# Kernel tuning notes

Hardware: AMD Instinct MI355X
Metric: run time of the kernel (lower is better)

## Reference

```python
import jax, jax.numpy as jnp
import numpy as np

B, W, D, R = 2, 1024, 1024, 16
GAMMA_FLOOR = 0.85


def setup_inputs() -> dict:
    key = jax.random.key(0)
    ks = jax.random.split(key, 8)
    h = jax.random.normal(ks[0], (B, W, D), jnp.float32)
    # faithful parameter initialization (as in __init__)
    gammas = jnp.linspace(0.95, 0.995, R)
    decay_logit = jnp.log(gammas / (1.0 - gammas))
    pos = jnp.arange(W, dtype=jnp.float32)
    causal = jnp.tril(jnp.ones((W, W), jnp.float32))
    dist0 = jnp.clip(pos[None, :] - pos[:, None], 0.0)  # (j - i)+ , used for k_base init
    k_init = jnp.exp(-0.15 * dist0) * causal
    k_base = k_init / jnp.clip(k_init.sum(axis=1, keepdims=True), 1e-8)
    u = jax.random.normal(ks[1], (D, R), jnp.float32) * 0.05
    v = jax.random.normal(ks[2], (D, R), jnp.float32) * 0.05
    proj_w = jax.random.normal(ks[3], (D, D), jnp.float32) * 0.02
    proj_b = jnp.zeros((D,), jnp.float32)
    up_w = jax.random.normal(ks[4], (D, 2 * D), jnp.float32) * 0.02
    up_b = jnp.zeros((2 * D,), jnp.float32)
    down_w = jax.random.normal(ks[5], (2 * D, D), jnp.float32) * 0.02
    down_b = jnp.zeros((D,), jnp.float32)
    return {
        'h': h,
        'decay_logit': decay_logit,
        'k_base': k_base,
        'k_base_gate_logit': jnp.asarray(8.0, jnp.float32),
        'u': u,
        'v': v,
        'alpha_logit': jnp.asarray(0.0, jnp.float32),
        'proj_w': proj_w,
        'proj_b': proj_b,
        'norm1_scale': jnp.ones((D,), jnp.float32),
        'norm2_scale': jnp.ones((D,), jnp.float32),
        'up_w': up_w,
        'up_b': up_b,
        'down_w': down_w,
        'down_b': down_b,
    }


def _rmsnorm(x, scale, eps=1e-8):
    return x / jnp.sqrt(jnp.mean(x * x, axis=-1, keepdims=True) + eps) * scale


def _l2norm(x, eps=1e-8):
    # matches F.normalize: x / max(||x||, eps)
    n = jnp.sqrt(jnp.sum(x * x, axis=-1, keepdims=True))
    return x / jnp.maximum(n, eps)


def reference(h, decay_logit, k_base, k_base_gate_logit, u, v, alpha_logit,
              proj_w, proj_b, norm1_scale, norm2_scale, up_w, up_b, down_w, down_b):
    b, w, d = h.shape
    pos = jnp.arange(w, dtype=h.dtype)
    causal = jnp.tril(jnp.ones((w, w), h.dtype))

    residual = h
    h_norm = _rmsnorm(h, norm1_scale)

    gate = jax.nn.sigmoid(k_base_gate_logit)
    kb = k_base[:w, :w] * causal * gate
    out = jnp.einsum('ij,bjd->bid', kb, h_norm)

    q = _l2norm(h_norm @ u)  # (b, w, r)
    k = _l2norm(h_norm @ v)  # (b, w, r)

    gamma = GAMMA_FLOOR + (1.0 - GAMMA_FLOOR) * jax.nn.sigmoid(decay_logit)  # (r,)
    alpha = jax.nn.sigmoid(alpha_logit)  # alpha_cap = 1.0

    # decay mask: exp((i-j)+ * log(gamma_r)) on causal entries -> (w, w, r)
    dist = jnp.clip(pos[:, None] - pos[None, :], 0.0)
    log_gamma = jnp.log(jnp.clip(gamma, 1e-8))
    decay_mask = jnp.exp(dist[:, :, None] * log_gamma[None, None, :]) * causal[:, :, None]

    kh = k[..., None] * h_norm[:, :, None, :]  # (b, w, r, d)
    causal_inner = jnp.einsum('ijr,bjrd->bird', decay_mask, kh)  # (b, w, r, d)
    out = out + alpha * jnp.einsum('bwr,bwrd->bwd', q, causal_inner)

    out = out @ proj_w + proj_b
    h2 = residual + out
    h2n = _rmsnorm(h2, norm2_scale)
    mlp = jax.nn.gelu(h2n @ up_w + up_b, approximate=False) @ down_w + down_b
    return h2 + mlp
```

## Files before the change

kernel.cpp:

```cpp
#include <hip/hip_runtime.h>

#define Bv 2
#define Wv 1024
#define Dv 1024
#define Rv 16

typedef __bf16 bf16;
typedef __attribute__((ext_vector_type(8))) __bf16 bf16x8;
typedef __attribute__((ext_vector_type(4))) __bf16 bf16x4;
typedef __attribute__((ext_vector_type(4))) float f32x4;

static __device__ __forceinline__ float sigmoidf_(float x) {
    return 1.0f / (1.0f + expf(-x));
}

static __device__ __forceinline__ void gload_lds16(const void* g, void* l) {
    __builtin_amdgcn_global_load_lds(
        (const __attribute__((address_space(1))) unsigned int*)g,
        (__attribute__((address_space(3))) unsigned int*)l, 16, 0, 0);
}

__global__ void rmsnorm_kernel(const float* __restrict__ x,
                               const float* __restrict__ scale,
                               bf16* __restrict__ outb) {
    int row = blockIdx.x;
    int t = threadIdx.x;
    float4 v = *(const float4*)(x + (size_t)row * Dv + t * 4);
    float ss = v.x * v.x + v.y * v.y + v.z * v.z + v.w * v.w;
    for (int off = 32; off > 0; off >>= 1) ss += __shfl_down(ss, off);
    __shared__ float wsum[4];
    __shared__ float inv_s;
    int lane = t & 63, wid = t >> 6;
    if (lane == 0) wsum[wid] = ss;
    __syncthreads();
    if (t == 0) {
        float tot = wsum[0] + wsum[1] + wsum[2] + wsum[3];
        inv_s = rsqrtf(tot * (1.0f / Dv) + 1e-8f);
    }
    __syncthreads();
    float inv = inv_s;
    float4 sc = *(const float4*)(scale + t * 4);
    bf16x4 ob = {(bf16)(v.x * inv * sc.x), (bf16)(v.y * inv * sc.y),
                 (bf16)(v.z * inv * sc.z), (bf16)(v.w * inv * sc.w)};
    *(bf16x4*)(outb + (size_t)row * Dv + t * 4) = ob;
}

__global__ void inv2_kernel(const bf16* __restrict__ x, float* __restrict__ inv2g) {
    int row = blockIdx.x;
    int t = threadIdx.x;
    bf16x4 vb = *(const bf16x4*)(x + (size_t)row * Dv + t * 4);
    float a0 = (float)vb[0], a1 = (float)vb[1], a2 = (float)vb[2], a3 = (float)vb[3];
    float ss = a0 * a0 + a1 * a1 + a2 * a2 + a3 * a3;
    for (int off = 32; off > 0; off >>= 1) ss += __shfl_down(ss, off);
    __shared__ float wsum[4];
    int lane = t & 63, wid = t >> 6;
    if (lane == 0) wsum[wid] = ss;
    __syncthreads();
    if (t == 0) {
        float tot = wsum[0] + wsum[1] + wsum[2] + wsum[3];
        inv2g[row] = rsqrtf(tot * (1.0f / Dv) + 1e-8f);
    }
}

__global__ void prep_kernel(const float* __restrict__ proj_w, const float* __restrict__ up_w,
                            const float* __restrict__ down_w,
                            const float* __restrict__ u, const float* __restrict__ v,
                            const float* __restrict__ n2,
                            const bf16* __restrict__ hnb,
                            bf16* __restrict__ proj_wT, bf16* __restrict__ up_wT,
                            bf16* __restrict__ down_wT, bf16* __restrict__ h_normT,
                            bf16* __restrict__ uvT) {
    __shared__ float tile[32][33];
    int blk = blockIdx.x;
    int t = threadIdx.x;
    if (blk >= 7168) {
        int i = (blk - 7168) * 256 + t;
        int rcol = i >> 10, d = i & (Wv - 1);
        float val = (rcol < Rv) ? u[(size_t)d * Rv + rcol] : v[(size_t)d * Rv + (rcol - Rv)];
        uvT[i] = (bf16)val;
        return;
    }
    const void* src;
    const float* rscale = nullptr;
    bf16* dst;
    int rows, cols, r0, c0;
    bool f32src = true;
    if (blk < 1024) {
        src = proj_w; dst = proj_wT; rows = 1024; cols = 1024;
        c0 = (blk & 31) * 32; r0 = (blk >> 5) * 32;
    } else if (blk < 3072) {
        int idx = blk - 1024;
        src = up_w; dst = up_wT; rows = 1024; cols = 2048; rscale = n2;
        c0 = (idx & 63) * 32; r0 = (idx >> 6) * 32;
    } else if (blk < 5120) {
        int idx = blk - 3072;
        src = down_w; dst = down_wT; rows = 2048; cols = 1024;
        c0 = (idx & 31) * 32; r0 = (idx >> 5) * 32;
    } else {
        int idx = blk - 5120;
        int b = idx >> 10; idx &= 1023;
        src = hnb + (size_t)b * Wv * Dv; dst = h_normT + (size_t)b * Dv * Wv;
        rows = 1024; cols = 1024; f32src = false;
        c0 = (idx & 31) * 32; r0 = (idx >> 5) * 32;
    }
    int r = t >> 3, c4 = (t & 7) * 4;
    float vv[4];
    if (f32src) {
        float4 x = *(const float4*)((const float*)src + (size_t)(r0 + r) * cols + c0 + c4);
        vv[0] = x.x; vv[1] = x.y; vv[2] = x.z; vv[3] = x.w;
    } else {
        bf16x4 x = *(const bf16x4*)((const bf16*)src + (size_t)(r0 + r) * cols + c0 + c4);
        vv[0] = (float)x[0]; vv[1] = (float)x[1]; vv[2] = (float)x[2]; vv[3] = (float)x[3];
    }
    float sc = rscale ? rscale[r0 + r] : 1.0f;
    tile[r][c4 + 0] = vv[0] * sc;
    tile[r][c4 + 1] = vv[1] * sc;
    tile[r][c4 + 2] = vv[2] * sc;
    tile[r][c4 + 3] = vv[3] * sc;
    __syncthreads();
    int n = t >> 3, k4 = (t & 7) * 4;
    bf16x4 ob = {(bf16)tile[k4 + 0][n], (bf16)tile[k4 + 1][n],
                 (bf16)tile[k4 + 2][n], (bf16)tile[k4 + 3][n]};
    *(bf16x4*)(dst + (size_t)(c0 + n) * rows + r0 + k4) = ob;
}

__global__ __launch_bounds__(256) void qk_mfma(
    const bf16* __restrict__ hnb,
    const bf16* __restrict__ uvT,
    const float* __restrict__ decay_logit,
    bf16* __restrict__ Qs, bf16* __restrict__ Ks) {
    int t = threadIdx.x, lane = t & 63, wid = t >> 6;
    int wm = wid >> 1, wn = wid & 1;
    int row0 = blockIdx.x * 32 + wm * 16;
    const bf16* Arow = hnb + (size_t)(row0 + (lane & 15)) * Dv + (lane >> 4) * 8;
    const bf16* Brow = uvT + (size_t)(wn * 16 + (lane & 15)) * Dv + (lane >> 4) * 8;
    f32x4 acc = {};
#pragma unroll 8
    for (int k0 = 0; k0 < Dv; k0 += 32) {
        bf16x8 a = *(const bf16x8*)(Arow + k0);
        bf16x8 b = *(const bf16x8*)(Brow + k0);
        acc = __builtin_amdgcn_mfma_f32_16x16x32_bf16(a, b, acc, 0, 0, 0);
    }
    int col = lane & 15;
    float dl = decay_logit[col];
    float gamma = 0.85f + 0.15f * sigmoidf_(dl);
    float logg = log2f(gamma);
#pragma unroll
    for (int r = 0; r < 4; ++r) {
        float vv = acc[r];
        float ss = vv * vv;
#pragma unroll
        for (int m = 1; m < 16; m <<= 1) ss += __shfl_xor(ss, m);
        float nrm = fmaxf(sqrtf(ss), 1e-8f);
        float val = vv / nrm;
        int grow = row0 + (lane >> 4) * 4 + r;
        int i = grow & (Wv - 1);
        if (wn == 0) {
            float pw = exp2f((float)i * logg);
            Qs[(size_t)grow * Rv + col] = (bf16)(val * pw);
        } else {
            float pwi = exp2f(-(float)i * logg);
            Ks[(size_t)grow * Rv + col] = (bf16)(val * pwi);
        }
    }
}

__global__ __launch_bounds__(256) void sbuild_mfma(
    const bf16* __restrict__ Qs, const bf16* __restrict__ Ks,
    const float* __restrict__ kbase,
    const float* __restrict__ gate_logit,
    const float* __restrict__ alpha_logit,
    bf16* __restrict__ S) {
    int it = blockIdx.y, jt = blockIdx.x;
    if (jt > it) return;
    int b = blockIdx.z;
    int t = threadIdx.x, lane = t & 63, wid = t >> 6;
    int wm = wid >> 1, wn = wid & 1;
    int i0 = it * 64, j0 = jt * 64;
    int l15 = lane & 15, chunk = lane >> 4;
    bf16x8 af[2], bfr[2];
    bf16x8 z8 = {};
#pragma unroll
    for (int mi = 0; mi < 2; ++mi)
        af[mi] = (chunk < 2)
            ? *(const bf16x8*)(Qs + (size_t)(b * Wv + i0 + wm * 32 + mi * 16 + l15) * Rv + chunk * 8)
            : z8;
#pragma unroll
    for (int ni = 0; ni < 2; ++ni)
        bfr[ni] = (chunk < 2)
            ? *(const bf16x8*)(Ks + (size_t)(b * Wv + j0 + wn * 32 + ni * 16 + l15) * Rv + chunk * 8)
            : z8;
    f32x4 acc[2][2] = {};
#pragma unroll
    for (int mi = 0; mi < 2; ++mi)
#pragma unroll
        for (int ni = 0; ni < 2; ++ni)
            acc[mi][ni] = __builtin_amdgcn_mfma_f32_16x16x32_bf16(af[mi], bfr[ni], acc[mi][ni], 0, 0, 0);
    float gate = sigmoidf_(gate_logit[0]);
    float alpha = sigmoidf_(alpha_logit[0]);
#pragma unroll
    for (int mi = 0; mi < 2; ++mi)
#pragma unroll
        for (int ni = 0; ni < 2; ++ni) {
            int j = j0 + wn * 32 + ni * 16 + l15;
#pragma unroll
            for (int r = 0; r < 4; ++r) {
                int i = i0 + wm * 32 + mi * 16 + chunk * 4 + r;
                float s = (j <= i) ? gate * kbase[(size_t)i * Wv + j] + alpha * acc[mi][ni][r] : 0.f;
                S[((size_t)b * Wv + i) * Wv + j] = (bf16)s;
            }
        }
}

template <bool GELU, bool OUT_BF16, int RES, bool CAUSAL, bool RS>
__global__ __launch_bounds__(256, 3) void mfma_gemm(
    const bf16* __restrict__ A, const bf16* __restrict__ Bt,
    const float* __restrict__ bias, const void* __restrict__ res,
    const float* __restrict__ rowscale,
    void* __restrict__ Cout, int M, int N, int K,
    long sA, long sB, long sC) {
    constexpr int BM = 64, BN = 64, BK = 128;
    __shared__ bf16 As[BM * BK];
    __shared__ bf16 Bs[BN * BK];

    const int gx = gridDim.x, gy = gridDim.y;
    int flat = blockIdx.x + gx * (blockIdx.y + gy * blockIdx.z);
    const int nwg = gx * gy * gridDim.z;
    const int cpx = nwg >> 3;
    int swz = (flat & 7) * cpx + (flat >> 3);
    const int bx = swz % gx;
    int tmp = swz / gx;
    const int by = tmp % gy;
    const int bz = tmp / gy;

    A += (size_t)bz * sA;
    Bt += (size_t)bz * sB;
    const int m0 = by * BM, n0 = bx * BN;
    const int t = threadIdx.x;
    const int lane = t & 63, wid = t >> 6;
    const int wm = wid >> 1, wn = wid & 1;
    f32x4 acc[2][2] = {};

    const int Klim = CAUSAL ? (m0 + BM < K ? m0 + BM : K) : K;

    const int srow = t >> 4;
    const int fcs = (t & 15) ^ (srow & 7);

    const int q = lane >> 4, s = lane & 7, l15 = lane & 15;

    for (int k0 = 0; k0 < Klim; k0 += BK) {
        __syncthreads();
#pragma unroll
        for (int it = 0; it < 4; ++it) {
            int r = srow + it * 16;
            gload_lds16(A + (size_t)(m0 + r) * K + k0 + fcs * 8,
                        As + it * 2048 + wid * 512);
        }
#pragma unroll
        for (int it = 0; it < 4; ++it) {
            int r = srow + it * 16;
            gload_lds16(Bt + (size_t)(n0 + r) * K + k0 + fcs * 8,
                        Bs + it * 2048 + wid * 512);
        }
        __syncthreads();

        bf16x8 af[2][4], bfr[2][4];
#pragma unroll
        for (int mi = 0; mi < 2; ++mi)
#pragma unroll
            for (int kk = 0; kk < 4; ++kk) {
                af[mi][kk] = *(const bf16x8*)&As[(wm * 32 + mi * 16 + l15) * BK + (((kk * 4 + q) ^ s) * 8)];
                bfr[mi][kk] = *(const bf16x8*)&Bs[(wn * 32 + mi * 16 + l15) * BK + (((kk * 4 + q) ^ s) * 8)];
            }
#pragma unroll
        for (int kk = 0; kk < 4; ++kk)
#pragma unroll
            for (int mi = 0; mi < 2; ++mi)
#pragma unroll
                for (int ni = 0; ni < 2; ++ni)
                    acc[mi][ni] = __builtin_amdgcn_mfma_f32_16x16x32_bf16(
                        af[mi][kk], bfr[ni][kk], acc[mi][ni], 0, 0, 0);
    }

    const int row_base = m0 + wm * 32;
    const int col_base = n0 + wn * 32;
#pragma unroll
    for (int mi = 0; mi < 2; ++mi) {
#pragma unroll
        for (int ni = 0; ni < 2; ++ni) {
            int col = col_base + ni * 16 + l15;
            float bv = bias ? bias[col] : 0.f;
#pragma unroll
            for (int r = 0; r < 4; ++r) {
                int row = row_base + mi * 16 + q * 4 + r;
                float val = acc[mi][ni][r];
                if (RS) val *= rowscale[row];
                val += bv;
                if (GELU) val = 0.5f * val * (1.0f + erff(val * 0.7071067811865476f));
                if (RES == 1)
                    val += ((const float*)res)[(size_t)bz * sC + (size_t)row * N + col];
                else if (RES == 2)
                    val += (float)((const bf16*)res)[(size_t)bz * sC + (size_t)row * N + col];
                if (OUT_BF16)
                    ((bf16*)Cout)[(size_t)bz * sC + (size_t)row * N + col] = (bf16)val;
                else
                    ((float*)Cout)[(size_t)bz * sC + (size_t)row * N + col] = val;
            }
        }
    }
}

extern "C" void kernel_launch(void* const* d_in, const int* in_sizes, int n_in,
                              void* d_out, int out_size, void* d_ws, size_t ws_size,
                              hipStream_t stream) {
    const float* h = (const float*)d_in[0];
    const float* decay_logit = (const float*)d_in[1];
    const float* k_base = (const float*)d_in[2];
    const float* gate_logit = (const float*)d_in[3];
    const float* u = (const float*)d_in[4];
    const float* v = (const float*)d_in[5];
    const float* alpha_logit = (const float*)d_in[6];
    const float* proj_w = (const float*)d_in[7];
    const float* proj_b = (const float*)d_in[8];
    const float* n1 = (const float*)d_in[9];
    const float* n2 = (const float*)d_in[10];
    const float* up_w = (const float*)d_in[11];
    const float* up_b = (const float*)d_in[12];
    const float* down_w = (const float*)d_in[13];
    const float* down_b = (const float*)d_in[14];
    float* out = (float*)d_out;

    char* ws = (char*)d_ws;
    bf16* hnb = (bf16*)ws;        ws += (size_t)Bv * Wv * Dv * 2;
    bf16* h_normT = (bf16*)ws;    ws += (size_t)Bv * Dv * Wv * 2;
    bf16* uvT = (bf16*)ws;        ws += (size_t)32 * Wv * 2;
    bf16* Qs = (bf16*)ws;         ws += (size_t)Bv * Wv * Rv * 2;
    bf16* Ks = (bf16*)ws;         ws += (size_t)Bv * Wv * Rv * 2;
    float* inv2g = (float*)ws;    ws += (size_t)Bv * Wv * 4;
    bf16* S = (bf16*)ws;          ws += (size_t)Bv * Wv * Wv * 2;
    bf16* out_s = (bf16*)ws;      ws += (size_t)Bv * Wv * Dv * 2;
    bf16* h2b = (bf16*)ws;        ws += (size_t)Bv * Wv * Dv * 2;
    bf16* g = (bf16*)ws;          ws += (size_t)Bv * Wv * 2 * Dv * 2;
    bf16* proj_wT = (bf16*)ws;    ws += (size_t)Dv * Dv * 2;
    bf16* up_wT = (bf16*)ws;      ws += (size_t)2 * Dv * Dv * 2;
    bf16* down_wT = (bf16*)ws;    ws += (size_t)2 * Dv * Dv * 2;

    int rows = Bv * Wv;

    rmsnorm_kernel<<<rows, 256, 0, stream>>>(h, n1, hnb);
    prep_kernel<<<7296, 256, 0, stream>>>(proj_w, up_w, down_w, u, v, n2, hnb,
                                          proj_wT, up_wT, down_wT, h_normT, uvT);
    qk_mfma<<<rows / 32, 256, 0, stream>>>(hnb, uvT, decay_logit, Qs, Ks);
    sbuild_mfma<<<dim3(Wv / 64, Wv / 64, Bv), 256, 0, stream>>>(
        Qs, Ks, k_base, gate_logit, alpha_logit, S);
    mfma_gemm<false, true, 0, true, false><<<dim3(Dv / 64, Wv / 64, Bv), 256, 0, stream>>>(
        S, h_normT, nullptr, nullptr, nullptr, out_s, Wv, Dv, Wv,
        (long)Wv * Wv, (long)Dv * Wv, (long)Wv * Dv);
    mfma_gemm<false, true, 1, false, false><<<dim3(Dv / 64, rows / 64, 1), 256, 0, stream>>>(
        out_s, proj_wT, proj_b, h, nullptr, h2b, rows, Dv, Dv, 0, 0, 0);
    inv2_kernel<<<rows, 256, 0, stream>>>(h2b, inv2g);
    mfma_gemm<true, true, 0, false, true><<<dim3(2 * Dv / 64, rows / 64, 1), 256, 0, stream>>>(
        h2b, up_wT, up_b, nullptr, inv2g, g, rows, 2 * Dv, Dv, 0, 0, 0);
    mfma_gemm<false, false, 2, false, false><<<dim3(Dv / 64, rows / 64, 1), 256, 0, stream>>>(
        g, down_wT, down_b, h2b, nullptr, out, rows, Dv, 2 * Dv, 0, 0, 0);
}
```

Before: 97.44 us.

## Use single-wave 64x64 GEMM blocks with double-buffered async LDS loads

Rewrites the shared GEMM kernel so each 64x64 output tile is computed by one 64-lane wavefront instead of four waves. The kernel now double-buffers LDS with BK=64 and prefetches two stages ahead using global_load_lds, replacing __syncthreads with explicit vmcnt/lgkmcnt waits. The aim is to overlap global loads with MFMA work and drop block-wide barriers. In exchange, each wave holds a 4x4 accumulator tile (more registers) and per-block parallelism falls to a quarter. The redundant reload of the last tile at the loop tail adds wasted loads.

```diff
diff --git a/kernel.cpp b/kernel.cpp
--- a/kernel.cpp
+++ b/kernel.cpp
@@ -213,15 +213,15 @@
 }
 
 template <bool GELU, bool OUT_BF16, int RES, bool CAUSAL, bool RS>
-__global__ __launch_bounds__(256, 3) void mfma_gemm(
+__global__ __launch_bounds__(64) void mfma_gemm(
     const bf16* __restrict__ A, const bf16* __restrict__ Bt,
     const float* __restrict__ bias, const void* __restrict__ res,
     const float* __restrict__ rowscale,
     void* __restrict__ Cout, int M, int N, int K,
     long sA, long sB, long sC) {
-    constexpr int BM = 64, BN = 64, BK = 128;
-    __shared__ bf16 As[BM * BK];
-    __shared__ bf16 Bs[BN * BK];
+    constexpr int BK = 64;
+    __shared__ bf16 As[2][64 * BK];
+    __shared__ bf16 Bs[2][64 * BK];
 
     const int gx = gridDim.x, gy = gridDim.y;
     int flat = blockIdx.x + gx * (blockIdx.y + gy * blockIdx.z);
@@ -235,64 +235,70 @@
 
     A += (size_t)bz * sA;
     Bt += (size_t)bz * sB;
-    const int m0 = by * BM, n0 = bx * BN;
+    const int m0 = by * 64, n0 = bx * 64;
     const int t = threadIdx.x;
-    const int lane = t & 63, wid = t >> 6;
-    const int wm = wid >> 1, wn = wid & 1;
-    f32x4 acc[2][2] = {};
-
-    const int Klim = CAUSAL ? (m0 + BM < K ? m0 + BM : K) : K;
-
-    const int srow = t >> 4;
-    const int fcs = (t & 15) ^ (srow & 7);
-
-    const int q = lane >> 4, s = lane & 7, l15 = lane & 15;
-
-    for (int k0 = 0; k0 < Klim; k0 += BK) {
-        __syncthreads();
-#pragma unroll
-        for (int it = 0; it < 4; ++it) {
-            int r = srow + it * 16;
-            gload_lds16(A + (size_t)(m0 + r) * K + k0 + fcs * 8,
-                        As + it * 2048 + wid * 512);
+
+    f32x4 acc[4][4] = {};
+
+    const int Klim = CAUSAL ? (m0 + 64 < K ? m0 + 64 : K) : K;
+    const int nt = Klim >> 6;
+
+    const int srow = t >> 3;
+    const int sg = (t & 7) ^ srow;
+    const bf16* Asrc = A + (size_t)(m0 + srow) * K + sg * 8;
+    const bf16* Bsrc = Bt + (size_t)(n0 + srow) * K + sg * 8;
+
+    const int q = t >> 4, s = t & 7, l15 = t & 15;
+
+#define STAGE(sb, kt)                                                          \
+    do {                                                                       \
+        const bf16* a_ = Asrc + (size_t)(kt) * BK;                             \
+        const bf16* b_ = Bsrc + (size_t)(kt) * BK;                             \
+        _Pragma("unroll") for (int it_ = 0; it_ < 8; ++it_) {                  \
+            gload_lds16(a_ + (size_t)it_ * 8 * K, &As[sb][it_ * 512]);         \
+            gload_lds16(b_ + (size_t)it_ * 8 * K, &Bs[sb][it_ * 512]);         \
+        }                                                                      \
+    } while (0)
+
+    STAGE(0, 0);
+    STAGE(1, nt > 1 ? 1 : 0);
+
+    for (int tt = 0; tt < nt; ++tt) {
+        const int cur = tt & 1;
+        asm volatile("s_waitcnt vmcnt(16)" ::: "memory");
+
+#pragma unroll
+        for (int kk = 0; kk < 2; ++kk) {
+            bf16x8 af[4], bfr[4];
+#pragma unroll
+            for (int mi = 0; mi < 4; ++mi)
+                af[mi] = *(const bf16x8*)&As[cur][(mi * 16 + l15) * BK + (((kk * 4 + q) ^ s) * 8)];
+#pragma unroll
+            for (int ni = 0; ni < 4; ++ni)
+                bfr[ni] = *(const bf16x8*)&Bs[cur][(ni * 16 + l15) * BK + (((kk * 4 + q) ^ s) * 8)];
+#pragma unroll
+            for (int mi = 0; mi < 4; ++mi)
+#pragma unroll
+                for (int ni = 0; ni < 4; ++ni)
+                    acc[mi][ni] = __builtin_amdgcn_mfma_f32_16x16x32_bf16(
+                        af[mi], bfr[ni], acc[mi][ni], 0, 0, 0);
         }
-#pragma unroll
-        for (int it = 0; it < 4; ++it) {
-            int r = srow + it * 16;
-            gload_lds16(Bt + (size_t)(n0 + r) * K + k0 + fcs * 8,
-                        Bs + it * 2048 + wid * 512);
-        }
-        __syncthreads();
-
-        bf16x8 af[2][4], bfr[2][4];
-#pragma unroll
-        for (int mi = 0; mi < 2; ++mi)
-#pragma unroll
-            for (int kk = 0; kk < 4; ++kk) {
-                af[mi][kk] = *(const bf16x8*)&As[(wm * 32 + mi * 16 + l15) * BK + (((kk * 4 + q) ^ s) * 8)];
-                bfr[mi][kk] = *(const bf16x8*)&Bs[(wn * 32 + mi * 16 + l15) * BK + (((kk * 4 + q) ^ s) * 8)];
-            }
-#pragma unroll
-        for (int kk = 0; kk < 4; ++kk)
-#pragma unroll
-            for (int mi = 0; mi < 2; ++mi)
-#pragma unroll
-                for (int ni = 0; ni < 2; ++ni)
-                    acc[mi][ni] = __builtin_amdgcn_mfma_f32_16x16x32_bf16(
-                        af[mi][kk], bfr[ni][kk], acc[mi][ni], 0, 0, 0);
-    }
-
-    const int row_base = m0 + wm * 32;
-    const int col_base = n0 + wn * 32;
-#pragma unroll
-    for (int mi = 0; mi < 2; ++mi) {
-#pragma unroll
-        for (int ni = 0; ni < 2; ++ni) {
-            int col = col_base + ni * 16 + l15;
+
+        asm volatile("s_waitcnt lgkmcnt(0)" ::: "memory");
+        int kn = (tt + 2 < nt) ? tt + 2 : nt - 1;
+        STAGE(cur, kn);
+    }
+#undef STAGE
+
+#pragma unroll
+    for (int mi = 0; mi < 4; ++mi) {
+#pragma unroll
+        for (int ni = 0; ni < 4; ++ni) {
+            int col = n0 + ni * 16 + l15;
             float bv = bias ? bias[col] : 0.f;
 #pragma unroll
             for (int r = 0; r < 4; ++r) {
-                int row = row_base + mi * 16 + q * 4 + r;
+                int row = m0 + mi * 16 + q * 4 + r;
                 float val = acc[mi][ni][r];
                 if (RS) val *= rowscale[row];
                 val += bv;
@@ -353,14 +359,14 @@
     qk_mfma<<<rows / 32, 256, 0, stream>>>(hnb, uvT, decay_logit, Qs, Ks);
     sbuild_mfma<<<dim3(Wv / 64, Wv / 64, Bv), 256, 0, stream>>>(
         Qs, Ks, k_base, gate_logit, alpha_logit, S);
-    mfma_gemm<false, true, 0, true, false><<<dim3(Dv / 64, Wv / 64, Bv), 256, 0, stream>>>(
+    mfma_gemm<false, true, 0, true, false><<<dim3(Dv / 64, Wv / 64, Bv), 64, 0, stream>>>(
         S, h_normT, nullptr, nullptr, nullptr, out_s, Wv, Dv, Wv,
         (long)Wv * Wv, (long)Dv * Wv, (long)Wv * Dv);
-    mfma_gemm<false, true, 1, false, false><<<dim3(Dv / 64, rows / 64, 1), 256, 0, stream>>>(
+    mfma_gemm<false, true, 1, false, false><<<dim3(Dv / 64, rows / 64, 1), 64, 0, stream>>>(
         out_s, proj_wT, proj_b, h, nullptr, h2b, rows, Dv, Dv, 0, 0, 0);
     inv2_kernel<<<rows, 256, 0, stream>>>(h2b, inv2g);
-    mfma_gemm<true, true, 0, false, true><<<dim3(2 * Dv / 64, rows / 64, 1), 256, 0, stream>>>(
+    mfma_gemm<true, true, 0, false, true><<<dim3(2 * Dv / 64, rows / 64, 1), 64, 0, stream>>>(
         h2b, up_wT, up_b, nullptr, inv2g, g, rows, 2 * Dv, Dv, 0, 0, 0);
-    mfma_gemm<false, false, 2, false, false><<<dim3(Dv / 64, rows / 64, 1), 256, 0, stream>>>(
+    mfma_gemm<false, false, 2, false, false><<<dim3(Dv / 64, rows / 64, 1), 64, 0, stream>>>(
         g, down_wT, down_b, h2b, nullptr, out, rows, Dv, 2 * Dv, 0, 0, 0);
 }
```

After: 134.2 us. 37.8% more time.

## Fuse S-matrix construction into causal GEMM and fuse RMSNorm reduction into epilogue

Applied to the files above, without the earlier changes.

Removes the separate kernel that materialised the full bf16 S matrix. The causal GEMM now computes each S tile on the fly from Q/K MFMAs and a bf16 copy of k_base, writing it straight into LDS. The second RMSNorm kernel is also dropped: the proj GEMM epilogue writes partial row sums of squares, and the up-projection GEMM reduces them into per-row inverse scales. This saves a 4 MB write and reread of S plus two launches. In exchange, S is recomputed by every column-tile block (16x redundant small MFMAs and k_base reads), and k_base is converted to bf16 in the prep kernel, which is extra precision loss.

```diff
diff --git a/kernel.cpp b/kernel.cpp
--- a/kernel.cpp
+++ b/kernel.cpp
@@ -45,34 +45,25 @@
     *(bf16x4*)(outb + (size_t)row * Dv + t * 4) = ob;
 }
 
-__global__ void inv2_kernel(const bf16* __restrict__ x, float* __restrict__ inv2g) {
-    int row = blockIdx.x;
-    int t = threadIdx.x;
-    bf16x4 vb = *(const bf16x4*)(x + (size_t)row * Dv + t * 4);
-    float a0 = (float)vb[0], a1 = (float)vb[1], a2 = (float)vb[2], a3 = (float)vb[3];
-    float ss = a0 * a0 + a1 * a1 + a2 * a2 + a3 * a3;
-    for (int off = 32; off > 0; off >>= 1) ss += __shfl_down(ss, off);
-    __shared__ float wsum[4];
-    int lane = t & 63, wid = t >> 6;
-    if (lane == 0) wsum[wid] = ss;
-    __syncthreads();
-    if (t == 0) {
-        float tot = wsum[0] + wsum[1] + wsum[2] + wsum[3];
-        inv2g[row] = rsqrtf(tot * (1.0f / Dv) + 1e-8f);
-    }
-}
-
 __global__ void prep_kernel(const float* __restrict__ proj_w, const float* __restrict__ up_w,
                             const float* __restrict__ down_w,
                             const float* __restrict__ u, const float* __restrict__ v,
                             const float* __restrict__ n2,
+                            const float* __restrict__ kbase,
                             const bf16* __restrict__ hnb,
                             bf16* __restrict__ proj_wT, bf16* __restrict__ up_wT,
                             bf16* __restrict__ down_wT, bf16* __restrict__ h_normT,
-                            bf16* __restrict__ uvT) {
+                            bf16* __restrict__ uvT, bf16* __restrict__ kbb) {
     __shared__ float tile[32][33];
     int blk = blockIdx.x;
     int t = threadIdx.x;
+    if (blk >= 7296) {
+        size_t base = (size_t)(blk - 7296) * 1024 + t * 4;
+        float4 x = *(const float4*)(kbase + base);
+        bf16x4 ob = {(bf16)x.x, (bf16)x.y, (bf16)x.z, (bf16)x.w};
+        *(bf16x4*)(kbb + base) = ob;
+        return;
+    }
     if (blk >= 7168) {
         int i = (blk - 7168) * 256 + t;
         int rcol = i >> 10, d = i & (Wv - 1);
@@ -165,63 +156,15 @@
     }
 }
 
-__global__ __launch_bounds__(256) void sbuild_mfma(
+__global__ __launch_bounds__(256, 3) void sgemm1(
     const bf16* __restrict__ Qs, const bf16* __restrict__ Ks,
-    const float* __restrict__ kbase,
-    const float* __restrict__ gate_logit,
-    const float* __restrict__ alpha_logit,
-    bf16* __restrict__ S) {
-    int it = blockIdx.y, jt = blockIdx.x;
-    if (jt > it) return;
-    int b = blockIdx.z;
-    int t = threadIdx.x, lane = t & 63, wid = t >> 6;
-    int wm = wid >> 1, wn = wid & 1;
-    int i0 = it * 64, j0 = jt * 64;
-    int l15 = lane & 15, chunk = lane >> 4;
-    bf16x8 af[2], bfr[2];
-    bf16x8 z8 = {};
-#pragma unroll
-    for (int mi = 0; mi < 2; ++mi)
-        af[mi] = (chunk < 2)
-            ? *(const bf16x8*)(Qs + (size_t)(b * Wv + i0 + wm * 32 + mi * 16 + l15) * Rv + chunk * 8)
-            : z8;
-#pragma unroll
-    for (int ni = 0; ni < 2; ++ni)
-        bfr[ni] = (chunk < 2)
-            ? *(const bf16x8*)(Ks + (size_t)(b * Wv + j0 + wn * 32 + ni * 16 + l15) * Rv + chunk * 8)
-            : z8;
-    f32x4 acc[2][2] = {};
-#pragma unroll
-    for (int mi = 0; mi < 2; ++mi)
-#pragma unroll
-        for (int ni = 0; ni < 2; ++ni)
-            acc[mi][ni] = __builtin_amdgcn_mfma_f32_16x16x32_bf16(af[mi], bfr[ni], acc[mi][ni], 0, 0, 0);
-    float gate = sigmoidf_(gate_logit[0]);
-    float alpha = sigmoidf_(alpha_logit[0]);
-#pragma unroll
-    for (int mi = 0; mi < 2; ++mi)
-#pragma unroll
-        for (int ni = 0; ni < 2; ++ni) {
-            int j = j0 + wn * 32 + ni * 16 + l15;
-#pragma unroll
-            for (int r = 0; r < 4; ++r) {
-                int i = i0 + wm * 32 + mi * 16 + chunk * 4 + r;
-                float s = (j <= i) ? gate * kbase[(size_t)i * Wv + j] + alpha * acc[mi][ni][r] : 0.f;
-                S[((size_t)b * Wv + i) * Wv + j] = (bf16)s;
-            }
-        }
-}
-
-template <bool GELU, bool OUT_BF16, int RES, bool CAUSAL, bool RS>
-__global__ __launch_bounds__(256, 3) void mfma_gemm(
-    const bf16* __restrict__ A, const bf16* __restrict__ Bt,
-    const float* __restrict__ bias, const void* __restrict__ res,
-    const float* __restrict__ rowscale,
-    void* __restrict__ Cout, int M, int N, int K,
-    long sA, long sB, long sC) {
-    constexpr int BM = 64, BN = 64, BK = 128;
-    __shared__ bf16 As[BM * BK];
-    __shared__ bf16 Bs[BN * BK];
+    const bf16* __restrict__ kbb,
+    const float* __restrict__ gate_logit, const float* __restrict__ alpha_logit,
+    const bf16* __restrict__ Bt,
+    bf16* __restrict__ Cout) {
+    constexpr int BK = 128;
+    __shared__ bf16 As[64 * BK];
+    __shared__ bf16 Bs[64 * BK];
 
     const int gx = gridDim.x, gy = gridDim.y;
     int flat = blockIdx.x + gx * (blockIdx.y + gy * blockIdx.z);
@@ -233,6 +176,125 @@
     const int by = tmp % gy;
     const int bz = tmp / gy;
 
+    const int m0 = by * 64;
+    const int n0 = bx * 64;
+    const int t = threadIdx.x;
+    const int lane = t & 63, wid = t >> 6;
+    const int wm = wid >> 1, wn = wid & 1;
+    const int q = lane >> 4, s = lane & 7, l15 = lane & 15;
+
+    const float gate = sigmoidf_(gate_logit[0]);
+    const float alpha = sigmoidf_(alpha_logit[0]);
+
+    bf16x8 z8 = {};
+    bf16x8 bq[4];
+#pragma unroll
+    for (int ib = 0; ib < 4; ++ib)
+        bq[ib] = (q < 2)
+            ? *(const bf16x8*)(Qs + (size_t)(bz * Wv + m0 + ib * 16 + l15) * Rv + q * 8)
+            : z8;
+
+    f32x4 acc[2][2] = {};
+    const int Klim = m0 + 64;
+
+    const int srow = t >> 4;
+    const int fcs = (t & 15) ^ (srow & 7);
+    const bf16* Bsrc = Bt + (size_t)bz * Dv * Wv;
+
+    for (int k0 = 0; k0 < Klim; k0 += BK) {
+        __syncthreads();
+
+        const int jb = k0 + wid * 32;
+        bf16x8 ak[2];
+#pragma unroll
+        for (int ja = 0; ja < 2; ++ja)
+            ak[ja] = (q < 2)
+                ? *(const bf16x8*)(Ks + (size_t)(bz * Wv + jb + ja * 16 + l15) * Rv + q * 8)
+                : z8;
+#pragma unroll
+        for (int ja = 0; ja < 2; ++ja) {
+#pragma unroll
+            for (int ib = 0; ib < 4; ++ib) {
+                f32x4 zz = {};
+                f32x4 sa = __builtin_amdgcn_mfma_f32_16x16x32_bf16(ak[ja], bq[ib], zz, 0, 0, 0);
+                int il = ib * 16 + l15;
+                int ii = m0 + il;
+                int jl = wid * 32 + ja * 16 + q * 4;
+                int jj = k0 + jl;
+                bf16x4 kv = *(const bf16x4*)(kbb + (size_t)ii * Wv + jj);
+                bf16x4 sv;
+#pragma unroll
+                for (int r = 0; r < 4; ++r) {
+                    float x = gate * (float)kv[r] + alpha * sa[r];
+                    sv[r] = (jj + r <= ii) ? (bf16)x : (bf16)0.f;
+                }
+                *(bf16x4*)((char*)As + il * 256 + (((jl >> 3) ^ (il & 7)) * 16) + (jl & 7) * 2) = sv;
+            }
+        }
+
+#pragma unroll
+        for (int it = 0; it < 4; ++it) {
+            int r = srow + it * 16;
+            gload_lds16(Bsrc + (size_t)(n0 + r) * Wv + k0 + fcs * 8,
+                        Bs + it * 2048 + wid * 512);
+        }
+        __syncthreads();
+
+        bf16x8 af[2][4], bfr[2][4];
+#pragma unroll
+        for (int mi = 0; mi < 2; ++mi)
+#pragma unroll
+            for (int kk = 0; kk < 4; ++kk) {
+                af[mi][kk] = *(const bf16x8*)&As[(wm * 32 + mi * 16 + l15) * BK + (((kk * 4 + q) ^ s) * 8)];
+                bfr[mi][kk] = *(const bf16x8*)&Bs[(wn * 32 + mi * 16 + l15) * BK + (((kk * 4 + q) ^ s) * 8)];
+            }
+#pragma unroll
+        for (int kk = 0; kk < 4; ++kk)
+#pragma unroll
+            for (int mi = 0; mi < 2; ++mi)
+#pragma unroll
+                for (int ni = 0; ni < 2; ++ni)
+                    acc[mi][ni] = __builtin_amdgcn_mfma_f32_16x16x32_bf16(
+                        af[mi][kk], bfr[ni][kk], acc[mi][ni], 0, 0, 0);
+    }
+
+    const int row_base = m0 + wm * 32;
+    const int col_base = n0 + wn * 32;
+#pragma unroll
+    for (int mi = 0; mi < 2; ++mi)
+#pragma unroll
+        for (int ni = 0; ni < 2; ++ni) {
+            int col = col_base + ni * 16 + l15;
+#pragma unroll
+            for (int r = 0; r < 4; ++r) {
+                int row = row_base + mi * 16 + q * 4 + r;
+                Cout[(size_t)bz * Wv * Dv + (size_t)row * Dv + col] = (bf16)acc[mi][ni][r];
+            }
+        }
+}
+
+template <bool GELU, bool OUT_BF16, int RES, bool CAUSAL, bool SSQW, bool SSQR>
+__global__ __launch_bounds__(256, 3) void mfma_gemm(
+    const bf16* __restrict__ A, const bf16* __restrict__ Bt,
+    const float* __restrict__ bias, const void* __restrict__ res,
+    float* __restrict__ ssqp,
+    void* __restrict__ Cout, int M, int N, int K,
+    long sA, long sB, long sC) {
+    constexpr int BM = 64, BN = 64, BK = 128;
+    __shared__ bf16 As[BM * BK];
+    __shared__ bf16 Bs[BN * BK];
+    __shared__ float sinv[64];
+
+    const int gx = gridDim.x, gy = gridDim.y;
+    int flat = blockIdx.x + gx * (blockIdx.y + gy * blockIdx.z);
+    const int nwg = gx * gy * gridDim.z;
+    const int cpx = nwg >> 3;
+    int swz = (flat & 7) * cpx + (flat >> 3);
+    const int bx = swz % gx;
+    int tmp = swz / gx;
+    const int by = tmp % gy;
+    const int bz = tmp / gy;
+
     A += (size_t)bz * sA;
     Bt += (size_t)bz * sB;
     const int m0 = by * BM, n0 = bx * BN;
@@ -241,11 +303,20 @@
     const int wm = wid >> 1, wn = wid & 1;
     f32x4 acc[2][2] = {};
 
+    if (SSQR) {
+        int rr = t >> 2, qt = t & 3;
+        const float4* pp = (const float4*)(ssqp + (size_t)(m0 + rr) * 32 + qt * 8);
+        float4 p0 = pp[0], p1 = pp[1];
+        float sm = p0.x + p0.y + p0.z + p0.w + p1.x + p1.y + p1.z + p1.w;
+        sm += __shfl_xor(sm, 1);
+        sm += __shfl_xor(sm, 2);
+        if (qt == 0) sinv[rr] = rsqrtf(sm * (1.0f / Dv) + 1e-8f);
+    }
+
     const int Klim = CAUSAL ? (m0 + BM < K ? m0 + BM : K) : K;
 
     const int srow = t >> 4;
     const int fcs = (t & 15) ^ (srow & 7);
-
     const int q = lane >> 4, s = lane & 7, l15 = lane & 15;
 
     for (int k0 = 0; k0 < Klim; k0 += BK) {
@@ -284,6 +355,13 @@
 
     const int row_base = m0 + wm * 32;
     const int col_base = n0 + wn * 32;
+    float ssq[2][4];
+    if (SSQW) {
+#pragma unroll
+        for (int mi = 0; mi < 2; ++mi)
+#pragma unroll
+            for (int r = 0; r < 4; ++r) ssq[mi][r] = 0.f;
+    }
 #pragma unroll
     for (int mi = 0; mi < 2; ++mi) {
 #pragma unroll
@@ -294,19 +372,34 @@
             for (int r = 0; r < 4; ++r) {
                 int row = row_base + mi * 16 + q * 4 + r;
                 float val = acc[mi][ni][r];
-                if (RS) val *= rowscale[row];
+                if (SSQR) val *= sinv[row - m0];
                 val += bv;
                 if (GELU) val = 0.5f * val * (1.0f + erff(val * 0.7071067811865476f));
                 if (RES == 1)
                     val += ((const float*)res)[(size_t)bz * sC + (size_t)row * N + col];
                 else if (RES == 2)
                     val += (float)((const bf16*)res)[(size_t)bz * sC + (size_t)row * N + col];
+                if (SSQW) ssq[mi][r] += val * val;
                 if (OUT_BF16)
                     ((bf16*)Cout)[(size_t)bz * sC + (size_t)row * N + col] = (bf16)val;
                 else
                     ((float*)Cout)[(size_t)bz * sC + (size_t)row * N + col] = val;
             }
         }
+    }
+    if (SSQW) {
+#pragma unroll
+        for (int mi = 0; mi < 2; ++mi)
+#pragma unroll
+            for (int r = 0; r < 4; ++r) {
+                float vsum = ssq[mi][r];
+                vsum += __shfl_xor(vsum, 1);
+                vsum += __shfl_xor(vsum, 2);
+                vsum += __shfl_xor(vsum, 4);
+                vsum += __shfl_xor(vsum, 8);
+                if (l15 == 0)
+                    ssqp[(size_t)(row_base + mi * 16 + q * 4 + r) * 32 + bx * 2 + wn] = vsum;
+            }
     }
 }
 
@@ -336,8 +429,8 @@
     bf16* uvT = (bf16*)ws;        ws += (size_t)32 * Wv * 2;
     bf16* Qs = (bf16*)ws;         ws += (size_t)Bv * Wv * Rv * 2;
     bf16* Ks = (bf16*)ws;         ws += (size_t)Bv * Wv * Rv * 2;
-    float* inv2g = (float*)ws;    ws += (size_t)Bv * Wv * 4;
-    bf16* S = (bf16*)ws;          ws += (size_t)Bv * Wv * Wv * 2;
+    bf16* kbb = (bf16*)ws;        ws += (size_t)Wv * Wv * 2;
+    float* ssqp = (float*)ws;     ws += (size_t)Bv * Wv * 32 * 4;
     bf16* out_s = (bf16*)ws;      ws += (size_t)Bv * Wv * Dv * 2;
     bf16* h2b = (bf16*)ws;        ws += (size_t)Bv * Wv * Dv * 2;
     bf16* g = (bf16*)ws;          ws += (size_t)Bv * Wv * 2 * Dv * 2;
@@ -348,19 +441,15 @@
     int rows = Bv * Wv;
 
     rmsnorm_kernel<<<rows, 256, 0, stream>>>(h, n1, hnb);
-    prep_kernel<<<7296, 256, 0, stream>>>(proj_w, up_w, down_w, u, v, n2, hnb,
-                                          proj_wT, up_wT, down_wT, h_normT, uvT);
+    prep_kernel<<<8320, 256, 0, stream>>>(proj_w, up_w, down_w, u, v, n2, k_base, hnb,
+                                          proj_wT, up_wT, down_wT, h_normT, uvT, kbb);
     qk_mfma<<<rows / 32, 256, 0, stream>>>(hnb, uvT, decay_logit, Qs, Ks);
-    sbuild_mfma<<<dim3(Wv / 64, Wv / 64, Bv), 256, 0, stream>>>(
-        Qs, Ks, k_base, gate_logit, alpha_logit, S);
-    mfma_gemm<false, true, 0, true, false><<<dim3(Dv / 64, Wv / 64, Bv), 256, 0, stream>>>(
-        S, h_normT, nullptr, nullptr, nullptr, out_s, Wv, Dv, Wv,
-        (long)Wv * Wv, (long)Dv * Wv, (long)Wv * Dv);
-    mfma_gemm<false, true, 1, false, false><<<dim3(Dv / 64, rows / 64, 1), 256, 0, stream>>>(
-        out_s, proj_wT, proj_b, h, nullptr, h2b, rows, Dv, Dv, 0, 0, 0);
-    inv2_kernel<<<rows, 256, 0, stream>>>(h2b, inv2g);
-    mfma_gemm<true, true, 0, false, true><<<dim3(2 * Dv / 64, rows / 64, 1), 256, 0, stream>>>(
-        h2b, up_wT, up_b, nullptr, inv2g, g, rows, 2 * Dv, Dv, 0, 0, 0);
-    mfma_gemm<false, false, 2, false, false><<<dim3(Dv / 64, rows / 64, 1), 256, 0, stream>>>(
-        g, down_wT, down_b, h2b, nullptr, out, rows, Dv, 2 * Dv, 0, 0, 0);
-}
+    sgemm1<<<dim3(Dv / 64, Wv / 64, Bv), 256, 0, stream>>>(
+        Qs, Ks, kbb, gate_logit, alpha_logit, h_normT, out_s);
+    mfma_gemm<false, true, 1, false, true, false><<<dim3(Dv / 64, rows / 64, 1), 256, 0, stream>>>(
+        out_s, proj_wT, proj_b, h, ssqp, h2b, rows, Dv, Dv, 0, 0, 0);
+    mfma_gemm<true, true, 0, false, false, true><<<dim3(2 * Dv / 64, rows / 64, 1), 256, 0, stream>>>(
+        h2b, up_wT, up_b, nullptr, ssqp, g, rows, 2 * Dv, Dv, 0, 0, 0);
+    mfma_gemm<false, false, 2, false, false, false><<<dim3(Dv / 64, rows / 64, 1), 256, 0, stream>>>(
+        g, down_wT, down_b, h2b, ssqp, out, rows, Dv, 2 * Dv, 0, 0, 0);
+}
```

Result: slower. 102.7 us (+5.4%).
